# Optimization experiments

Hardware: AMD Instinct MI355X
Metric: run time of the kernel (lower is better)

The kernel has to match this reference:

```python
import jax, jax.numpy as jnp
import numpy as np

DIM = 256
HID = 1024
BATCH = 16384
STEP_SIZE = 0.1
NSTEPS = 10  # int(1.0 / step_size)


def setup_inputs() -> dict:
    key = jax.random.key(0)
    ks = jax.random.split(key, 8)
    x = jax.random.normal(ks[0], (BATCH, DIM), dtype=jnp.float32)
    # Scaled init so tanh layers stay in a sane range (like default torch init).
    W1 = jax.random.normal(ks[1], (DIM + 1, HID), dtype=jnp.float32) / np.sqrt(DIM + 1)
    b1 = jnp.zeros((HID,), dtype=jnp.float32)
    W2 = jax.random.normal(ks[2], (HID, HID), dtype=jnp.float32) / np.sqrt(HID)
    b2 = jnp.zeros((HID,), dtype=jnp.float32)
    W3 = jax.random.normal(ks[3], (HID, DIM), dtype=jnp.float32) / np.sqrt(HID)
    b3 = jnp.zeros((DIM,), dtype=jnp.float32)
    proj_mat = jax.random.normal(ks[4], (DIM, DIM), dtype=jnp.float32)
    return {"x": x, "W1": W1, "b1": b1, "W2": W2, "b2": b2,
            "W3": W3, "b3": b3, "proj_mat": proj_mat}


def reference(x, W1, b1, W2, b2, W3, b3, proj_mat):
    """FlowProposal.log_prob: backward RK4 integration of dx/dt = v(x,t)
    from t=1 to t=0 with Hutchinson trace estimation via forward-mode JVP.
    Returns log q(x), shape [batch]."""
    dtype = x.dtype

    def net(xc, t):
        # VelocityMLP: concat(x, t) -> tanh MLP -> velocity [B, DIM]
        tcol = jnp.broadcast_to(jnp.asarray(t, dtype), (xc.shape[0], 1))
        h = jnp.tanh(jnp.concatenate([xc, tcol], axis=1) @ W1 + b1)
        h = jnp.tanh(h @ W2 + b2)
        return h @ W3 + b3

    # Deterministic hashed Hutchinson noise (from the INITIAL x, as in torch).
    noise = jnp.sin((x @ proj_mat) * 1000.0) * 1.41421356  # sqrt(2)

    def dyn(xc, t):
        v, jv = jax.jvp(lambda xi: net(xi, t), (xc,), (noise,))
        tr = jnp.sum(noise * jv, axis=1, keepdims=True)  # eps^T J eps, [B,1]
        return v, tr

    dt = -STEP_SIZE

    def step(carry, k):
        xt, ljt = carry
        t = 1.0 + dt * k
        v1, tr1 = dyn(xt, t)
        v2, tr2 = dyn(xt + dt * 0.5 * v1, t + dt * 0.5)
        v3, tr3 = dyn(xt + dt * 0.5 * v2, t + dt * 0.5)
        v4, tr4 = dyn(xt + dt * v3, t + dt)
        xt = xt + (dt / 6.0) * (v1 + 2 * v2 + 2 * v3 + v4)
        ljt = ljt + (dt / 6.0) * (tr1 + 2 * tr2 + 2 * tr3 + tr4)
        return (xt, ljt), None

    init = (x, jnp.zeros((x.shape[0], 1), dtype))
    (xt, ljt), _ = jax.lax.scan(step, init, jnp.arange(NSTEPS, dtype=dtype))

    log_prob_z = -0.5 * jnp.sum(xt * xt, axis=1) - 0.5 * DIM * jnp.log(jnp.asarray(2.0 * np.pi, dtype))
    return log_prob_z - ljt[:, 0]
```

## Files before the change

kernel.cpp:

```cpp
#include <hip/hip_runtime.h>
#include <stdint.h>
#include <stddef.h>

typedef unsigned short ushort_t;
typedef float f32x4 __attribute__((ext_vector_type(4)));
typedef short short8 __attribute__((ext_vector_type(8)));

#define NB 16384
#define DIMX 256
#define HIDX 1024
#define DTC (-0.1f)

__device__ __forceinline__ unsigned short f2bf_bits(float f){
  unsigned int u = __float_as_uint(f);
  unsigned int r = (u + 0x7FFFu + ((u >> 16) & 1u)) >> 16;
  return (unsigned short)r;
}
__device__ __forceinline__ float bf2f_bits(unsigned short s){
  return __uint_as_float(((unsigned int)s) << 16);
}
__device__ __forceinline__ float fast_tanh(float x){
  float a = fabsf(x);
  float e = __expf(a + a);
  float r = 1.0f - 2.0f / (e + 1.0f);
  return copysignf(r, x);
}
__device__ __forceinline__ void gload16(const void* g, void* l){
  __builtin_amdgcn_global_load_lds(
      (const __attribute__((address_space(1))) void*)g,
      (__attribute__((address_space(3))) void*)l, 16, 0, 0);
}
template<int N> __device__ __forceinline__ void wait_vmcnt(){
  if constexpr (N == 0)      asm volatile("s_waitcnt vmcnt(0)" ::: "memory");
  else if constexpr (N == 4) asm volatile("s_waitcnt vmcnt(4)" ::: "memory");
  else if constexpr (N == 6) asm volatile("s_waitcnt vmcnt(6)" ::: "memory");
  else if constexpr (N == 8) asm volatile("s_waitcnt vmcnt(8)" ::: "memory");
  else if constexpr (N == 12) asm volatile("s_waitcnt vmcnt(12)" ::: "memory");
  else if constexpr (N == 16) asm volatile("s_waitcnt vmcnt(16)" ::: "memory");
  else static_assert(N == 0, "unsupported vmcnt");
}
__device__ __forceinline__ int ldsx(int r, int c){
  return r * 64 + (c ^ ((r & 7) << 3));
}

__global__ void prep_weights(const float* __restrict__ W1, const float* __restrict__ W2,
                             const float* __restrict__ W3,
                             ushort_t* __restrict__ W1at, ushort_t* __restrict__ W2t,
                             ushort_t* __restrict__ W3t, ushort_t* __restrict__ W3n){
  int i = blockIdx.x * blockDim.x + threadIdx.x;
  const int T1 = 1024 * 256, T2 = 1024 * 1024, T3 = 256 * 1024, T4 = 1024 * 256;
  if (i < T1){
    int n = i >> 8, k = i & 255;
    W1at[i] = f2bf_bits(W1[k * 1024 + n]);
  } else if (i < T1 + T2){
    int j = i - T1; int n = j >> 10, k = j & 1023;
    W2t[j] = f2bf_bits(W2[k * 1024 + n]);
  } else if (i < T1 + T2 + T3){
    int j = i - T1 - T2; int n = j >> 10, k = j & 1023;
    W3t[j] = f2bf_bits(W3[k * 256 + n]);
  } else if (i < T1 + T2 + T3 + T4){
    int j = i - T1 - T2 - T3;
    W3n[j] = f2bf_bits(W3[j]);
  }
}

__global__ void noise_init(const float* __restrict__ x, const float* __restrict__ proj,
                           ushort_t* __restrict__ noise_bf,
                           float* __restrict__ xt, ushort_t* __restrict__ xcbf,
                           float* __restrict__ ljt){
  const int r0 = blockIdx.x * 8;
  const int j = threadIdx.x;
  __shared__ float xrow[8][256];
  #pragma unroll
  for (int r = 0; r < 8; ++r) xrow[r][j] = x[(size_t)(r0 + r) * 256 + j];
  __syncthreads();
  float s[8] = {0.f,0.f,0.f,0.f,0.f,0.f,0.f,0.f};
  for (int k = 0; k < 256; ++k){
    float p = proj[k * 256 + j];
    #pragma unroll
    for (int r = 0; r < 8; ++r) s[r] = fmaf(xrow[r][k], p, s[r]);
  }
  #pragma unroll
  for (int r = 0; r < 8; ++r){
    float nz = sinf(s[r] * 1000.0f) * 1.41421356237f;
    size_t idx = (size_t)(r0 + r) * 256 + j;
    noise_bf[idx] = f2bf_bits(nz);
    float xv = xrow[r][j];
    xt[idx] = xv;
    xcbf[idx] = f2bf_bits(xv);
  }
  if (j < 8) ljt[r0 + j] = 0.0f;
}

template<int BM, int BN, int WGM, int K, int DUAL, int EPI, int PIPE>
__launch_bounds__(512, 2)
__global__ void gemm_kernel(const ushort_t* __restrict__ A1, const ushort_t* __restrict__ A2,
                            const ushort_t* __restrict__ Wt,
                            ushort_t* __restrict__ out1, ushort_t* __restrict__ out2,
                            const float* __restrict__ bias, const float* __restrict__ w1trow,
                            float tval,
                            const ushort_t* __restrict__ dz1,
                            const ushort_t* __restrict__ gtr,
                            float* __restrict__ xt, float* __restrict__ vacc,
                            ushort_t* __restrict__ xcbf,
                            float* __restrict__ ljt, float wdt6, int rk){
  constexpr int BK = 64;
  constexpr int WGN = 8 / WGM;
  constexpr int WM = BM / WGM, WN = BN / WGN;
  constexpr int M_REP = WM / 16, N_REP = WN / 16;
  constexpr int ATILES = DUAL ? 2 : 1;
  constexpr int CH_A = BM / 8;
  constexpr int CH_TOT = ATILES * CH_A + BN / 8;
  constexpr int CH_PW = CH_TOT / 8;
  constexpr int BUF_E = (ATILES * BM + BN) * BK;
  constexpr int NBUF = PIPE ? 2 : 1;
  constexpr int NK = K / BK;
  static_assert(!PIPE || NK >= 2, "pipeline needs >=2 K-steps");

  __shared__ __align__(16) ushort_t lds[NBUF * BUF_E];

  const int m0 = blockIdx.x * BM;
  const int n0 = blockIdx.y * BN;
  const int tid = threadIdx.x;
  const int lane = tid & 63;
  const int wid = tid >> 6;
  const int wr = wid / WGN;
  const int wc = wid % WGN;

  f32x4 acc1[M_REP][N_REP] = {};
  f32x4 acc2[M_REP][N_REP] = {};

  const int srow = lane >> 3;
  const int scol = ((lane & 7) ^ srow) * 8;

  const ushort_t* srcb[CH_PW];
  #pragma unroll
  for (int c = 0; c < CH_PW; ++c){
    const int ch = wid * CH_PW + c;
    if (ch < CH_A)
      srcb[c] = A1 + (size_t)(m0 + ch * 8 + srow) * K + scol;
    else if (DUAL && ch < 2 * CH_A)
      srcb[c] = A2 + (size_t)(m0 + (ch - CH_A) * 8 + srow) * K + scol;
    else
      srcb[c] = Wt + (size_t)(n0 + (ch - ATILES * CH_A) * 8 + srow) * K + scol;
  }

  auto do_stage = [&](int buf, int ks){
    ushort_t* dst = lds + buf * BUF_E + (wid * CH_PW) * 512;
    const int k0 = ks * BK;
    #pragma unroll
    for (int c = 0; c < CH_PW; ++c)
      gload16(srcb[c] + k0, dst + c * 512);
  };

  auto compute = [&](int buf){
    const ushort_t* ldsA1 = lds + buf * BUF_E;
    const ushort_t* ldsA2 = ldsA1 + BM * BK;
    const ushort_t* ldsB  = ldsA1 + ATILES * BM * BK;
    #pragma unroll
    for (int kk = 0; kk < 2; ++kk){
      short8 a1f[M_REP], a2f[M_REP], bfr[N_REP];
      const int lco = kk * 32 + (lane >> 4) * 8;
      const int lro = lane & 15;
      #pragma unroll
      for (int m = 0; m < M_REP; ++m){
        int r = wr * WM + m * 16 + lro;
        a1f[m] = *(const short8*)(ldsA1 + ldsx(r, lco));
        if (DUAL) a2f[m] = *(const short8*)(ldsA2 + ldsx(r, lco));
      }
      #pragma unroll
      for (int n = 0; n < N_REP; ++n){
        int cN = wc * WN + n * 16 + lro;
        bfr[n] = *(const short8*)(ldsB + ldsx(cN, lco));
      }
      #pragma unroll
      for (int m = 0; m < M_REP; ++m){
        #pragma unroll
        for (int n = 0; n < N_REP; ++n){
          acc1[m][n] = __builtin_amdgcn_mfma_f32_16x16x32_bf16(a1f[m], bfr[n], acc1[m][n], 0, 0, 0);
          if (DUAL)
            acc2[m][n] = __builtin_amdgcn_mfma_f32_16x16x32_bf16(a2f[m], bfr[n], acc2[m][n], 0, 0, 0);
        }
      }
    }
  };

  if constexpr (PIPE){
    do_stage(0, 0);
    do_stage(1, 1);
    for (int ks = 0; ks < NK - 2; ++ks){
      wait_vmcnt<CH_PW>();
      __builtin_amdgcn_s_barrier();
      compute(ks & 1);
      asm volatile("s_waitcnt lgkmcnt(0)" ::: "memory");
      __builtin_amdgcn_s_barrier();
      do_stage(ks & 1, ks + 2);
    }
    wait_vmcnt<CH_PW>();
    __builtin_amdgcn_s_barrier();
    compute(NK & 1);
    wait_vmcnt<0>();
    __builtin_amdgcn_s_barrier();
    compute((NK - 1) & 1);
  } else {
    for (int ks = 0; ks < NK; ++ks){
      do_stage(0, ks);
      __syncthreads();
      compute(0);
      __syncthreads();
    }
  }

  const int rbase = (lane >> 4) * 4;
  const int cbase = lane & 15;
  if (EPI <= 1){
    #pragma unroll
    for (int m = 0; m < M_REP; ++m){
      #pragma unroll
      for (int n = 0; n < N_REP; ++n){
        #pragma unroll
        for (int j = 0; j < 4; ++j){
          const int R = m0 + wr * WM + m * 16 + rbase + j;
          const int C = n0 + wc * WN + n * 16 + cbase;
          const size_t idx = (size_t)R * HIDX + C;
          float a = acc1[m][n][j];
          if (EPI == 0){
            out1[idx] = f2bf_bits(a);
          } else {
            float z = a + bias[C] + tval * w1trow[C];
            float h = fast_tanh(z);
            out1[idx] = f2bf_bits(h);
            float d = bf2f_bits(dz1[idx]);
            out2[idx] = f2bf_bits(fmaf(-h, h, 1.0f) * d);
          }
        }
      }
    }
  } else if (EPI == 2){
    #pragma unroll
    for (int m = 0; m < M_REP; ++m){
      #pragma unroll
      for (int j = 0; j < 4; ++j){
        const int R = m0 + wr * WM + m * 16 + rbase + j;
        float psum = 0.0f;
        #pragma unroll
        for (int n = 0; n < N_REP; ++n){
          const int C = n0 + wc * WN + n * 16 + cbase;
          const size_t idx = (size_t)R * HIDX + C;
          float h = fast_tanh(acc1[m][n][j] + bias[C]);
          out1[idx] = f2bf_bits(h);
          float dh2 = fmaf(-h, h, 1.0f) * acc2[m][n][j];
          psum += dh2 * bf2f_bits(gtr[idx]);
        }
        #pragma unroll
        for (int off = 1; off < 16; off <<= 1) psum += __shfl_xor(psum, off, 64);
        if (cbase == 0) atomicAdd(&ljt[R], wdt6 * psum);
      }
    }
  } else {
    #pragma unroll
    for (int m = 0; m < M_REP; ++m){
      #pragma unroll
      for (int n = 0; n < N_REP; ++n){
        #pragma unroll
        for (int j = 0; j < 4; ++j){
          const int R = m0 + wr * WM + m * 16 + rbase + j;
          const int C = n0 + wc * WN + n * 16 + cbase;
          const size_t idx = (size_t)R * DIMX + C;
          float v = acc1[m][n][j] + bias[C];
          float xtv = xt[idx];
          if (rk == 0){
            vacc[idx] = v;
            xcbf[idx] = f2bf_bits(xtv + 0.5f * DTC * v);
          } else if (rk == 1){
            vacc[idx] += 2.0f * v;
            xcbf[idx] = f2bf_bits(xtv + 0.5f * DTC * v);
          } else if (rk == 2){
            vacc[idx] += 2.0f * v;
            xcbf[idx] = f2bf_bits(xtv + DTC * v);
          } else {
            float xtn = xtv + (DTC / 6.0f) * (vacc[idx] + v);
            xt[idx] = xtn;
            xcbf[idx] = f2bf_bits(xtn);
          }
        }
      }
    }
  }
}

__global__ void final_kernel(const float* __restrict__ xt, const float* __restrict__ ljt,
                             float* __restrict__ out){
  const int row = blockIdx.x * 4 + (threadIdx.x >> 6);
  const int lane = threadIdx.x & 63;
  const float4 xv = *(const float4*)(xt + (size_t)row * 256 + lane * 4);
  float s = xv.x * xv.x + xv.y * xv.y + xv.z * xv.z + xv.w * xv.w;
  #pragma unroll
  for (int off = 32; off; off >>= 1) s += __shfl_xor(s, off, 64);
  if (lane == 0) out[row] = -0.5f * s - 235.2482645f - ljt[row];
}

extern "C" void kernel_launch(void* const* d_in, const int* in_sizes, int n_in,
                              void* d_out, int out_size, void* d_ws, size_t ws_size,
                              hipStream_t stream){
  (void)in_sizes; (void)n_in; (void)out_size; (void)ws_size;
  const float* x    = (const float*)d_in[0];
  const float* W1   = (const float*)d_in[1];
  const float* b1   = (const float*)d_in[2];
  const float* W2   = (const float*)d_in[3];
  const float* b2   = (const float*)d_in[4];
  const float* W3   = (const float*)d_in[5];
  const float* b3   = (const float*)d_in[6];
  const float* proj = (const float*)d_in[7];

  size_t off = 0;
  char* wsb = (char*)d_ws;
  auto carve = [&](size_t n) -> char* {
    char* p = wsb + off; off += (n + 255) & ~(size_t)255; return p;
  };
  ushort_t* W1at     = (ushort_t*)carve((size_t)1024 * 256 * 2);
  ushort_t* W2t      = (ushort_t*)carve((size_t)1024 * 1024 * 2);
  ushort_t* W3t      = (ushort_t*)carve((size_t)256 * 1024 * 2);
  ushort_t* W3n      = (ushort_t*)carve((size_t)1024 * 256 * 2);
  ushort_t* noise_bf = (ushort_t*)carve((size_t)NB * 256 * 2);
  ushort_t* dz1      = (ushort_t*)carve((size_t)NB * 1024 * 2);
  ushort_t* gtr      = (ushort_t*)carve((size_t)NB * 1024 * 2);
  float*    xt       = (float*)carve((size_t)NB * 256 * 4);
  ushort_t* xcbf     = (ushort_t*)carve((size_t)NB * 256 * 2);
  float*    vacc     = (float*)carve((size_t)NB * 256 * 4);
  float*    ljt      = (float*)carve((size_t)NB * 4);
  ushort_t* h1       = (ushort_t*)carve((size_t)NB * 1024 * 2);
  ushort_t* dh1      = (ushort_t*)carve((size_t)NB * 1024 * 2);
  ushort_t* h2       = (ushort_t*)carve((size_t)NB * 1024 * 2);

  prep_weights<<<7168, 256, 0, stream>>>(W1, W2, W3, W1at, W2t, W3t, W3n);
  noise_init<<<NB / 8, 256, 0, stream>>>(x, proj, noise_bf, xt, xcbf, ljt);

  gemm_kernel<256, 256, 2, 256, 0, 0, 0><<<dim3(NB / 256, 4), 512, 0, stream>>>(
      noise_bf, nullptr, W1at, dz1, nullptr, nullptr, nullptr, 0.f,
      nullptr, nullptr, nullptr, nullptr, nullptr, nullptr, 0.f, 0);
  gemm_kernel<256, 256, 2, 256, 0, 0, 0><<<dim3(NB / 256, 4), 512, 0, stream>>>(
      noise_bf, nullptr, W3n, gtr, nullptr, nullptr, nullptr, 0.f,
      nullptr, nullptr, nullptr, nullptr, nullptr, nullptr, 0.f, 0);

  const float toff[4] = {0.0f, -0.05f, -0.05f, -0.1f};
  const float wst[4]  = {1.0f, 2.0f, 2.0f, 1.0f};
  for (int k = 0; k < 10; ++k){
    float t = 1.0f - 0.1f * (float)k;
    for (int s = 0; s < 4; ++s){
      gemm_kernel<256, 256, 2, 256, 0, 1, 0><<<dim3(NB / 256, 4), 512, 0, stream>>>(
          xcbf, nullptr, W1at, h1, dh1, b1, W1 + 256 * 1024, t + toff[s],
          dz1, nullptr, nullptr, nullptr, nullptr, nullptr, 0.f, 0);
      gemm_kernel<128, 256, 2, 1024, 1, 2, 1><<<dim3(NB / 128, 4), 512, 0, stream>>>(
          h1, dh1, W2t, h2, nullptr, b2, nullptr, 0.f,
          nullptr, gtr, nullptr, nullptr, nullptr, ljt, wst[s] * (DTC / 6.0f), 0);
      gemm_kernel<128, 128, 4, 1024, 0, 3, 0><<<dim3(NB / 128, 2), 512, 0, stream>>>(
          h2, nullptr, W3t, nullptr, nullptr, b3, nullptr, 0.f,
          nullptr, nullptr, xt, vacc, xcbf, nullptr, 0.f, s);
    }
  }
  final_kernel<<<NB / 4, 256, 0, stream>>>(xt, ljt, (float*)d_out);
}
```

Baseline: 5.639 ms.

## Use 4-stage BK=32 LDS pipeline with one barrier per step in dual W2 GEMM

Replaces the double-buffered BK=64 pipeline of the dual-input 1024x1024 GEMM with a four-buffer ring of BK=32 slices. It keeps three loads in flight and uses a single barrier per iteration, issuing the next prefetch after the LDS fragment reads. It adds a new XOR swizzle for 32-wide rows and raises wave priority around the MFMA block. The goal is to hide global-to-LDS latency and cut barrier stalls in the dominant GEMM, at the cost of a different LDS footprint (4*512*32 bf16 = 128KB) that may limit occupancy to one block per CU.

```diff
diff --git a/kernel.cpp b/kernel.cpp
--- a/kernel.cpp
+++ b/kernel.cpp
@@ -33,14 +33,14 @@
 template<int N> __device__ __forceinline__ void wait_vmcnt(){
   if constexpr (N == 0)      asm volatile("s_waitcnt vmcnt(0)" ::: "memory");
   else if constexpr (N == 4) asm volatile("s_waitcnt vmcnt(4)" ::: "memory");
-  else if constexpr (N == 6) asm volatile("s_waitcnt vmcnt(6)" ::: "memory");
   else if constexpr (N == 8) asm volatile("s_waitcnt vmcnt(8)" ::: "memory");
-  else if constexpr (N == 12) asm volatile("s_waitcnt vmcnt(12)" ::: "memory");
-  else if constexpr (N == 16) asm volatile("s_waitcnt vmcnt(16)" ::: "memory");
   else static_assert(N == 0, "unsupported vmcnt");
 }
 __device__ __forceinline__ int ldsx(int r, int c){
   return r * 64 + (c ^ ((r & 7) << 3));
+}
+__device__ __forceinline__ int ldsx2(int r, int g){
+  return r * 32 + ((g ^ ((r >> 1) & 3)) << 3);
 }
 
 __global__ void prep_weights(const float* __restrict__ W1, const float* __restrict__ W2,
@@ -104,20 +104,11 @@
                             float* __restrict__ xt, float* __restrict__ vacc,
                             ushort_t* __restrict__ xcbf,
                             float* __restrict__ ljt, float wdt6, int rk){
-  constexpr int BK = 64;
   constexpr int WGN = 8 / WGM;
   constexpr int WM = BM / WGM, WN = BN / WGN;
   constexpr int M_REP = WM / 16, N_REP = WN / 16;
   constexpr int ATILES = DUAL ? 2 : 1;
-  constexpr int CH_A = BM / 8;
-  constexpr int CH_TOT = ATILES * CH_A + BN / 8;
-  constexpr int CH_PW = CH_TOT / 8;
-  constexpr int BUF_E = (ATILES * BM + BN) * BK;
-  constexpr int NBUF = PIPE ? 2 : 1;
-  constexpr int NK = K / BK;
-  static_assert(!PIPE || NK >= 2, "pipeline needs >=2 K-steps");
-
-  __shared__ __align__(16) ushort_t lds[NBUF * BUF_E];
+  constexpr int ROWS = ATILES * BM + BN;
 
   const int m0 = blockIdx.x * BM;
   const int n0 = blockIdx.y * BN;
@@ -130,49 +121,56 @@
   f32x4 acc1[M_REP][N_REP] = {};
   f32x4 acc2[M_REP][N_REP] = {};
 
-  const int srow = lane >> 3;
-  const int scol = ((lane & 7) ^ srow) * 8;
-
-  const ushort_t* srcb[CH_PW];
-  #pragma unroll
-  for (int c = 0; c < CH_PW; ++c){
-    const int ch = wid * CH_PW + c;
-    if (ch < CH_A)
-      srcb[c] = A1 + (size_t)(m0 + ch * 8 + srow) * K + scol;
-    else if (DUAL && ch < 2 * CH_A)
-      srcb[c] = A2 + (size_t)(m0 + (ch - CH_A) * 8 + srow) * K + scol;
-    else
-      srcb[c] = Wt + (size_t)(n0 + (ch - ATILES * CH_A) * 8 + srow) * K + scol;
-  }
-
-  auto do_stage = [&](int buf, int ks){
-    ushort_t* dst = lds + buf * BUF_E + (wid * CH_PW) * 512;
-    const int k0 = ks * BK;
-    #pragma unroll
-    for (int c = 0; c < CH_PW; ++c)
-      gload16(srcb[c] + k0, dst + c * 512);
-  };
-
-  auto compute = [&](int buf){
-    const ushort_t* ldsA1 = lds + buf * BUF_E;
-    const ushort_t* ldsA2 = ldsA1 + BM * BK;
-    const ushort_t* ldsB  = ldsA1 + ATILES * BM * BK;
-    #pragma unroll
-    for (int kk = 0; kk < 2; ++kk){
+  if constexpr (PIPE == 2){
+    constexpr int NT = K / 32;
+    constexpr int CH = ROWS / 16;
+    constexpr int CH_PW = CH / 8;
+    constexpr int BUF_E = ROWS * 32;
+    static_assert(CH_PW * 8 == CH, "chunk split");
+    __shared__ __align__(16) ushort_t lds[4 * BUF_E];
+
+    const int srow = lane >> 2;
+    const int scol = (((lane & 3) ^ ((srow >> 1) & 3)) << 3);
+    const ushort_t* srcb[CH_PW];
+    #pragma unroll
+    for (int c = 0; c < CH_PW; ++c){
+      const int ch = wid * CH_PW + c;
+      const int r = ch * 16 + srow;
+      if (r < BM)            srcb[c] = A1 + (size_t)(m0 + r) * K + scol;
+      else if (DUAL && r < 2 * BM) srcb[c] = A2 + (size_t)(m0 + r - BM) * K + scol;
+      else                   srcb[c] = Wt + (size_t)(n0 + r - ATILES * BM) * K + scol;
+    }
+    auto do_stage = [&](int t){
+      ushort_t* dst = lds + (t & 3) * BUF_E + (wid * CH_PW) * 512;
+      #pragma unroll
+      for (int c = 0; c < CH_PW; ++c)
+        gload16(srcb[c] + t * 32, dst + c * 512);
+    };
+
+    do_stage(0); do_stage(1); do_stage(2);
+    const int g = lane >> 4;
+    const int lro = lane & 15;
+    for (int t = 0; t < NT; ++t){
+      asm volatile("s_waitcnt lgkmcnt(0)" ::: "memory");
+      __builtin_amdgcn_s_barrier();
+      if (t < NT - 2)       wait_vmcnt<8>();
+      else if (t == NT - 2) wait_vmcnt<4>();
+      else                  wait_vmcnt<0>();
+      const ushort_t* base = lds + (t & 3) * BUF_E;
       short8 a1f[M_REP], a2f[M_REP], bfr[N_REP];
-      const int lco = kk * 32 + (lane >> 4) * 8;
-      const int lro = lane & 15;
       #pragma unroll
       for (int m = 0; m < M_REP; ++m){
         int r = wr * WM + m * 16 + lro;
-        a1f[m] = *(const short8*)(ldsA1 + ldsx(r, lco));
-        if (DUAL) a2f[m] = *(const short8*)(ldsA2 + ldsx(r, lco));
+        a1f[m] = *(const short8*)(base + ldsx2(r, g));
+        if (DUAL) a2f[m] = *(const short8*)(base + ldsx2(BM + r, g));
       }
       #pragma unroll
       for (int n = 0; n < N_REP; ++n){
-        int cN = wc * WN + n * 16 + lro;
-        bfr[n] = *(const short8*)(ldsB + ldsx(cN, lco));
-      }
+        int cN = ATILES * BM + wc * WN + n * 16 + lro;
+        bfr[n] = *(const short8*)(base + ldsx2(cN, g));
+      }
+      if (t + 3 < NT) do_stage(t + 3);
+      __builtin_amdgcn_s_setprio(1);
       #pragma unroll
       for (int m = 0; m < M_REP; ++m){
         #pragma unroll
@@ -182,31 +180,67 @@
             acc2[m][n] = __builtin_amdgcn_mfma_f32_16x16x32_bf16(a2f[m], bfr[n], acc2[m][n], 0, 0, 0);
         }
       }
-    }
-  };
-
-  if constexpr (PIPE){
-    do_stage(0, 0);
-    do_stage(1, 1);
-    for (int ks = 0; ks < NK - 2; ++ks){
-      wait_vmcnt<CH_PW>();
-      __builtin_amdgcn_s_barrier();
-      compute(ks & 1);
-      asm volatile("s_waitcnt lgkmcnt(0)" ::: "memory");
-      __builtin_amdgcn_s_barrier();
-      do_stage(ks & 1, ks + 2);
-    }
-    wait_vmcnt<CH_PW>();
-    __builtin_amdgcn_s_barrier();
-    compute(NK & 1);
-    wait_vmcnt<0>();
-    __builtin_amdgcn_s_barrier();
-    compute((NK - 1) & 1);
+      __builtin_amdgcn_s_setprio(0);
+    }
   } else {
+    constexpr int BK = 64;
+    constexpr int CH_A = BM / 8;
+    constexpr int CH_TOT = ATILES * CH_A + BN / 8;
+    constexpr int CH_PW = CH_TOT / 8;
+    constexpr int BUF_E = ROWS * BK;
+    constexpr int NK = K / BK;
+    __shared__ __align__(16) ushort_t lds[BUF_E];
+
+    const int srow = lane >> 3;
+    const int scol = ((lane & 7) ^ srow) * 8;
+    const ushort_t* srcb[CH_PW];
+    #pragma unroll
+    for (int c = 0; c < CH_PW; ++c){
+      const int ch = wid * CH_PW + c;
+      if (ch < CH_A)
+        srcb[c] = A1 + (size_t)(m0 + ch * 8 + srow) * K + scol;
+      else if (DUAL && ch < 2 * CH_A)
+        srcb[c] = A2 + (size_t)(m0 + (ch - CH_A) * 8 + srow) * K + scol;
+      else
+        srcb[c] = Wt + (size_t)(n0 + (ch - ATILES * CH_A) * 8 + srow) * K + scol;
+    }
     for (int ks = 0; ks < NK; ++ks){
-      do_stage(0, ks);
+      {
+        ushort_t* dst = lds + (wid * CH_PW) * 512;
+        #pragma unroll
+        for (int c = 0; c < CH_PW; ++c)
+          gload16(srcb[c] + ks * BK, dst + c * 512);
+      }
       __syncthreads();
-      compute(0);
+      const ushort_t* ldsA1 = lds;
+      const ushort_t* ldsA2 = lds + BM * BK;
+      const ushort_t* ldsB  = lds + ATILES * BM * BK;
+      #pragma unroll
+      for (int kk = 0; kk < 2; ++kk){
+        short8 a1f[M_REP], a2f[M_REP], bfr[N_REP];
+        const int lco = kk * 32 + (lane >> 4) * 8;
+        const int lro = lane & 15;
+        #pragma unroll
+        for (int m = 0; m < M_REP; ++m){
+          int r = wr * WM + m * 16 + lro;
+          a1f[m] = *(const short8*)(ldsA1 + ldsx(r, lco));
+          if (DUAL) a2f[m] = *(const short8*)(ldsA2 + ldsx(r, lco));
+        }
+        #pragma unroll
+        for (int n = 0; n < N_REP; ++n){
+          int cN = wc * WN + n * 16 + lro;
+          bfr[n] = *(const short8*)(ldsB + ldsx(cN, lco));
+        }
+        #pragma unroll
+        for (int m = 0; m < M_REP; ++m){
+          #pragma unroll
+          for (int n = 0; n < N_REP; ++n){
+            acc1[m][n] = __builtin_amdgcn_mfma_f32_16x16x32_bf16(a1f[m], bfr[n], acc1[m][n], 0, 0, 0);
+            if (DUAL)
+              acc2[m][n] = __builtin_amdgcn_mfma_f32_16x16x32_bf16(a2f[m], bfr[n], acc2[m][n], 0, 0, 0);
+          }
+        }
+      }
       __syncthreads();
     }
   }
@@ -351,7 +385,7 @@
       gemm_kernel<256, 256, 2, 256, 0, 1, 0><<<dim3(NB / 256, 4), 512, 0, stream>>>(
           xcbf, nullptr, W1at, h1, dh1, b1, W1 + 256 * 1024, t + toff[s],
           dz1, nullptr, nullptr, nullptr, nullptr, nullptr, 0.f, 0);
-      gemm_kernel<128, 256, 2, 1024, 1, 2, 1><<<dim3(NB / 128, 4), 512, 0, stream>>>(
+      gemm_kernel<128, 256, 2, 1024, 1, 2, 2><<<dim3(NB / 128, 4), 512, 0, stream>>>(
           h1, dh1, W2t, h2, nullptr, b2, nullptr, 0.f,
           nullptr, gtr, nullptr, nullptr, nullptr, ljt, wst[s] * (DTC / 6.0f), 0);
       gemm_kernel<128, 128, 4, 1024, 0, 3, 0><<<dim3(NB / 128, 2), 512, 0, stream>>>(
```

New measurement: 6.015 ms. 1.07x slower.
